# Optimization experiments

Hardware: AMD Instinct MI355X
Metric: run time of the kernel (lower is better)

Reference implementation:

```python
import jax, jax.numpy as jnp
import numpy as np

N_NODES = 50000
N_EDGES = 800000
N_ENTS = 200000
N_RELS = 500
D = 128


def setup_inputs() -> dict:
    key = jax.random.key(0)
    ks = jax.random.split(key, 9)
    return {
        "prev_ent_embs": jax.random.normal(ks[0], (N_ENTS, D), dtype=jnp.float32),
        "rel_embs": jax.random.normal(ks[1], (N_RELS, D), dtype=jnp.float32),
        "loop_weight": jax.random.normal(ks[2], (D, D), dtype=jnp.float32) * 0.1,
        "evolve_loop_weight": jax.random.normal(ks[3], (D, D), dtype=jnp.float32) * 0.1,
        "weight_neighbor": jax.random.normal(ks[4], (D, D), dtype=jnp.float32) * 0.1,
        "node_id": jax.random.randint(ks[5], (N_NODES,), 0, N_ENTS, dtype=jnp.int64) if jax.config.jax_enable_x64 else jax.random.randint(ks[5], (N_NODES,), 0, N_ENTS, dtype=jnp.int32),
        "src": jax.random.randint(ks[6], (N_EDGES,), 0, N_NODES, dtype=jnp.int32),
        "dst": jax.random.randint(ks[7], (N_EDGES,), 0, N_NODES, dtype=jnp.int32),
        "etype": jax.random.randint(ks[8], (N_EDGES,), 0, N_RELS, dtype=jnp.int32),
    }


def reference(prev_ent_embs, rel_embs, loop_weight, evolve_loop_weight,
              weight_neighbor, node_id, src, dst, etype):
    n_nodes = node_id.shape[0]
    # node features gathered from global entity table
    h = prev_ent_embs[node_id]                                    # [N, D]

    # per-edge message: (h[src] + rel[type]) @ W_neighbor
    msg = (h[src] + rel_embs[etype]) @ weight_neighbor            # [E, D]

    # scatter-sum into destination nodes
    agg = jax.ops.segment_sum(msg, dst, num_segments=n_nodes)     # [N, D]

    # in-degree and norm (apply_func: h * in_norm, standard 1/in_degree)
    deg = jax.ops.segment_sum(jnp.ones_like(dst, dtype=h.dtype), dst,
                              num_segments=n_nodes)               # [N]
    has_in = deg > 0
    in_norm = jnp.where(has_in, 1.0 / jnp.maximum(deg, 1.0), 0.0)[:, None]
    agg = agg * in_norm

    # self-loop: loop_weight where in_degree>0, evolve_loop_weight otherwise
    loop_msg = jnp.where(has_in[:, None], h @ loop_weight, h @ evolve_loop_weight)

    # activation (dropout=0 -> identity in eval)
    return jax.nn.relu(agg + loop_msg)
```

## Files before the change

### kernel.cpp

```cpp
#include <hip/hip_runtime.h>
#include <hip/hip_bf16.h>
#include <stdint.h>

#define N_NODES 50000
#define N_EDGES 800000
#define N_ENTS  200000
#define N_RELS  500
#define DIM     128

#define DEGS 32
#define CAP  64

#define ZERO_REC ((int)(50000u | (500u << 16)))

using f32x4  = __attribute__((ext_vector_type(4))) float;
using bf16x8 = __attribute__((ext_vector_type(8))) short;

static __device__ __forceinline__ ushort f_to_bf16(float f) {
    __hip_bfloat16 h = __float2bfloat16(f);
    return *reinterpret_cast<ushort*>(&h);
}
static __device__ __forceinline__ uint pack2(float a, float b) {
    return (uint)f_to_bf16(a) | ((uint)f_to_bf16(b) << 16);
}
static __device__ __forceinline__ float blo(uint u) { return __uint_as_float(u << 16); }
static __device__ __forceinline__ float bhi(uint u) { return __uint_as_float(u & 0xffff0000u); }

__global__ __launch_bounds__(256) void k_front(
        const float* __restrict__ prev, const int* __restrict__ node_id,
        ushort* __restrict__ afull,
        const int* __restrict__ dst, const int* __restrict__ src,
        const int* __restrict__ etype,
        int* __restrict__ deg, uint* __restrict__ srcpk,
        const float* __restrict__ rel, ushort* __restrict__ rel_bf,
        const float* __restrict__ Wn, const float* __restrict__ Wl,
        ushort* __restrict__ WfT) {
    int blk = blockIdx.x;
    if (blk < 3125) {
        int e = blk * 256 + threadIdx.x;
        if (e < N_EDGES) {
            int dn = dst[e];
            uint rec = (uint)src[e] | ((uint)etype[e] << 16);
            int r = atomicAdd(&deg[dn * DEGS], 1);
            if (r < CAP) srcpk[dn * CAP + r] = rec;
        }
    } else if (blk < 6250) {
        int i = (blk - 3125) * 256 + threadIdx.x;
        int row = i >> 4, c = (i & 15) * 8;
        int nid = node_id[row];
        const float* p = prev + (size_t)nid * DIM + c;
        float4 v0 = *(const float4*)p;
        float4 v1 = *(const float4*)(p + 4);
        uint4 w;
        w.x = pack2(v0.x, v0.y);
        w.y = pack2(v0.z, v0.w);
        w.z = pack2(v1.x, v1.y);
        w.w = pack2(v1.z, v1.w);
        *(uint4*)(afull + (size_t)row * 256 + 128 + c) = w;
    } else if (blk < 6504) {
        int i = (blk - 6250) * 256 + threadIdx.x;
        if (i < 128 * 256) {
            int n = i >> 8, k = i & 255;
            float v = (k < 128) ? Wn[k * 128 + n] : Wl[(k - 128) * 128 + n];
            WfT[i] = f_to_bf16(v);
        } else {
            int j = i - 128 * 256;
            if (j < N_RELS * 64) {
                float2 v = *(const float2*)(rel + j * 2);
                *(uint*)(rel_bf + j * 2) = pack2(v.x, v.y);
            }
        }
    } else {
        int t = threadIdx.x;
        if (t < 128)       ((uint*)(afull + (size_t)50000 * 256))[t] = 0u;
        else if (t < 192)  ((uint*)(rel_bf + 500 * 128))[t - 128]    = 0u;
    }
}

__global__ __launch_bounds__(256) void k_agg(ushort* __restrict__ afull,
                                             const ushort* __restrict__ rel_bf,
                                             const uint* __restrict__ srcpk,
                                             const int* __restrict__ deg) {
    int wave = threadIdx.x >> 6, lane = threadIdx.x & 63;
    int n = blockIdx.x * 4 + wave;
    if (n >= N_NODES) return;
    int d = deg[n * DEGS];
    int cnt = min(d, CAP);
    int g = lane >> 4, q = lane & 15;
    const ushort* hb = afull + 128 + q * 8;
    const ushort* rb = rel_bf + q * 8;
    float acc[8] = {0.f, 0.f, 0.f, 0.f, 0.f, 0.f, 0.f, 0.f};

#define ACC4(hv, rv)                                              \
    acc[0] += blo(hv.x) + blo(rv.x); acc[1] += bhi(hv.x) + bhi(rv.x); \
    acc[2] += blo(hv.y) + blo(rv.y); acc[3] += bhi(hv.y) + bhi(rv.y); \
    acc[4] += blo(hv.z) + blo(rv.z); acc[5] += bhi(hv.z) + bhi(rv.z); \
    acc[6] += blo(hv.w) + blo(rv.w); acc[7] += bhi(hv.w) + bhi(rv.w);

    int rec = (lane < cnt) ? (int)srcpk[n * CAP + lane] : ZERO_REC;
    for (int j = 0; j < cnt; j += 8) {
        uint e0 = (uint)__shfl(rec, j + g);
        uint e1 = (uint)__shfl(rec, j + 4 + g);
        uint4 h0 = *(const uint4*)(hb + (size_t)(e0 & 0xffffu) * 256);
        uint4 r0 = *(const uint4*)(rb + (e0 >> 16) * 128);
        uint4 h1 = *(const uint4*)(hb + (size_t)(e1 & 0xffffu) * 256);
        uint4 r1 = *(const uint4*)(rb + (e1 >> 16) * 128);
        ACC4(h0, r0);
        ACC4(h1, r1);
    }
#undef ACC4

#pragma unroll
    for (int i = 0; i < 8; i++) {
        acc[i] += __shfl_xor(acc[i], 16);
        acc[i] += __shfl_xor(acc[i], 32);
    }
    float norm = (d > 0) ? 1.0f / (float)d : 0.0f;
    if (g == 0) {
        uint4 w;
        w.x = pack2(acc[0] * norm, acc[1] * norm);
        w.y = pack2(acc[2] * norm, acc[3] * norm);
        w.z = pack2(acc[4] * norm, acc[5] * norm);
        w.w = pack2(acc[6] * norm, acc[7] * norm);
        *(uint4*)(afull + (size_t)n * 256 + q * 8) = w;
    }
}

#define LDSK 264
__global__ __launch_bounds__(256) void k_mm(const ushort* __restrict__ afull,
                                            const ushort* __restrict__ WfT,
                                            float* __restrict__ out) {
    __shared__ ushort wl[128 * LDSK];
    for (int idx = threadIdx.x; idx < 128 * 32; idx += 256) {
        int n = idx >> 5, p = idx & 31;
        uint4 v = *(const uint4*)(WfT + n * 256 + p * 8);
        *(uint4*)(&wl[n * LDSK + p * 8]) = v;
    }
    __syncthreads();

    int wave = threadIdx.x >> 6, lane = threadIdx.x & 63;
    int m = lane & 15, quad = lane >> 4;
    int rowBase = blockIdx.x * 128 + wave * 32;

    f32x4 acc[2][8];
#pragma unroll
    for (int rt = 0; rt < 2; rt++)
#pragma unroll
        for (int ct = 0; ct < 8; ct++) acc[rt][ct] = f32x4{0.f, 0.f, 0.f, 0.f};

    int r0 = rowBase + m;      if (r0 > N_NODES - 1) r0 = N_NODES - 1;
    int r1 = rowBase + 16 + m; if (r1 > N_NODES - 1) r1 = N_NODES - 1;
    const ushort* pa0 = afull + (size_t)r0 * 256 + quad * 8;
    const ushort* pa1 = afull + (size_t)r1 * 256 + quad * 8;

#pragma unroll
    for (int ks = 0; ks < 8; ks++) {
        bf16x8 a0 = *(const bf16x8*)(pa0 + ks * 32);
        bf16x8 a1 = *(const bf16x8*)(pa1 + ks * 32);
#pragma unroll
        for (int ct = 0; ct < 8; ct++) {
            bf16x8 b = *(const bf16x8*)(&wl[(ct * 16 + m) * LDSK + ks * 32 + quad * 8]);
            acc[0][ct] = __builtin_amdgcn_mfma_f32_16x16x32_bf16(a0, b, acc[0][ct], 0, 0, 0);
            acc[1][ct] = __builtin_amdgcn_mfma_f32_16x16x32_bf16(a1, b, acc[1][ct], 0, 0, 0);
        }
    }

#pragma unroll
    for (int rt = 0; rt < 2; rt++) {
        int rbase = rowBase + rt * 16 + quad * 4;
#pragma unroll
        for (int reg = 0; reg < 4; reg++) {
            int grow = rbase + reg;
            if (grow < N_NODES) {
#pragma unroll
                for (int ct = 0; ct < 8; ct++) {
                    float v = acc[rt][ct][reg];
                    out[(size_t)grow * 128 + ct * 16 + m] = v > 0.f ? v : 0.f;
                }
            }
        }
    }
}

__global__ __launch_bounds__(256) void k_fixup(const ushort* __restrict__ afull,
                                               const float* __restrict__ We,
                                               const int* __restrict__ deg,
                                               float* __restrict__ out) {
    int n = blockIdx.x * 256 + threadIdx.x;
    if (n >= N_NODES) return;
    if (deg[n * DEGS] != 0) return;
    for (int c = 0; c < 128; c++) {
        float a = 0.f;
        for (int k = 0; k < 128; k++) {
            float h = blo((uint)afull[(size_t)n * 256 + 128 + k]);
            a += h * We[k * 128 + c];
        }
        out[(size_t)n * 128 + c] = a > 0.f ? a : 0.f;
    }
}

extern "C" void kernel_launch(void* const* d_in, const int* in_sizes, int n_in,
                              void* d_out, int out_size, void* d_ws, size_t ws_size,
                              hipStream_t stream) {
    const float* prev  = (const float*)d_in[0];
    const float* rel   = (const float*)d_in[1];
    const float* Wl    = (const float*)d_in[2];
    const float* We    = (const float*)d_in[3];
    const float* Wn    = (const float*)d_in[4];
    const int* node_id = (const int*)d_in[5];
    const int* src     = (const int*)d_in[6];
    const int* dst     = (const int*)d_in[7];
    const int* etype   = (const int*)d_in[8];
    float* out = (float*)d_out;

    char* ws = (char*)d_ws;
    ushort* afull  = (ushort*)(ws);
    ushort* WfT    = (ushort*)(ws + 25600512);
    ushort* rel_bf = (ushort*)(ws + 25666048);
    int* deg       = (int*)(ws + 25794304);
    uint* srcpk    = (uint*)(ws + 32194304);

    hipMemsetAsync(deg, 0, 6400000, stream);
    k_front <<<6505,  256, 0, stream>>>(prev, node_id, afull, dst, src, etype,
                                        deg, srcpk, rel, rel_bf, Wn, Wl, WfT);
    k_agg   <<<12500, 256, 0, stream>>>(afull, rel_bf, srcpk, deg);
    k_mm    <<<391,   256, 0, stream>>>(afull, WfT, out);
    k_fixup <<<196,   256, 0, stream>>>(afull, We, deg, out);
}
```

Measured before the change: 242.2 us.

## Assign one node per 16-lane group in aggregation and fold fixup into matmul

The aggregation kernel now gives each 16-lane group its own destination node, so four nodes share a wave instead of one. Edge records are loaded in chunks of 16, which removes the cross-group shuffle reduction. The separate zero-in-degree fixup kernel is merged into the matmul launch as extra blocks, saving one kernel launch, and the matmul skips writing rows with no in-edges. The cost is uneven work inside a wave, since each group loops for its own node's degree, and the fixup blocks still run a slow scalar loop alongside the matmul blocks.

```diff
diff --git a/kernel.cpp b/kernel.cpp
--- a/kernel.cpp
+++ b/kernel.cpp
@@ -82,54 +82,66 @@
                                              const uint* __restrict__ srcpk,
                                              const int* __restrict__ deg) {
     int wave = threadIdx.x >> 6, lane = threadIdx.x & 63;
-    int n = blockIdx.x * 4 + wave;
-    if (n >= N_NODES) return;
+    int g = lane >> 4, q = lane & 15;
+    int n = blockIdx.x * 16 + wave * 4 + g;
     int d = deg[n * DEGS];
     int cnt = min(d, CAP);
-    int g = lane >> 4, q = lane & 15;
     const ushort* hb = afull + 128 + q * 8;
     const ushort* rb = rel_bf + q * 8;
     float acc[8] = {0.f, 0.f, 0.f, 0.f, 0.f, 0.f, 0.f, 0.f};
 
-#define ACC4(hv, rv)                                              \
+#define ACC4(hv, rv)                                                  \
     acc[0] += blo(hv.x) + blo(rv.x); acc[1] += bhi(hv.x) + bhi(rv.x); \
     acc[2] += blo(hv.y) + blo(rv.y); acc[3] += bhi(hv.y) + bhi(rv.y); \
     acc[4] += blo(hv.z) + blo(rv.z); acc[5] += bhi(hv.z) + bhi(rv.z); \
     acc[6] += blo(hv.w) + blo(rv.w); acc[7] += bhi(hv.w) + bhi(rv.w);
 
-    int rec = (lane < cnt) ? (int)srcpk[n * CAP + lane] : ZERO_REC;
-    for (int j = 0; j < cnt; j += 8) {
-        uint e0 = (uint)__shfl(rec, j + g);
-        uint e1 = (uint)__shfl(rec, j + 4 + g);
-        uint4 h0 = *(const uint4*)(hb + (size_t)(e0 & 0xffffu) * 256);
-        uint4 r0 = *(const uint4*)(rb + (e0 >> 16) * 128);
-        uint4 h1 = *(const uint4*)(hb + (size_t)(e1 & 0xffffu) * 256);
-        uint4 r1 = *(const uint4*)(rb + (e1 >> 16) * 128);
-        ACC4(h0, r0);
-        ACC4(h1, r1);
+    for (int b = 0; b < cnt; b += 16) {
+        int rec = (b + q < cnt) ? (int)srcpk[n * CAP + b + q] : ZERO_REC;
+        int jmax = min(16, cnt - b);
+        for (int j = 0; j < jmax; j += 2) {
+            uint e0 = (uint)__shfl(rec, (g << 4) + j);
+            uint e1 = (uint)__shfl(rec, (g << 4) + j + 1);
+            uint4 h0 = *(const uint4*)(hb + (size_t)(e0 & 0xffffu) * 256);
+            uint4 r0 = *(const uint4*)(rb + (e0 >> 16) * 128);
+            uint4 h1 = *(const uint4*)(hb + (size_t)(e1 & 0xffffu) * 256);
+            uint4 r1 = *(const uint4*)(rb + (e1 >> 16) * 128);
+            ACC4(h0, r0);
+            ACC4(h1, r1);
+        }
     }
 #undef ACC4
 
-#pragma unroll
-    for (int i = 0; i < 8; i++) {
-        acc[i] += __shfl_xor(acc[i], 16);
-        acc[i] += __shfl_xor(acc[i], 32);
-    }
     float norm = (d > 0) ? 1.0f / (float)d : 0.0f;
-    if (g == 0) {
-        uint4 w;
-        w.x = pack2(acc[0] * norm, acc[1] * norm);
-        w.y = pack2(acc[2] * norm, acc[3] * norm);
-        w.z = pack2(acc[4] * norm, acc[5] * norm);
-        w.w = pack2(acc[6] * norm, acc[7] * norm);
-        *(uint4*)(afull + (size_t)n * 256 + q * 8) = w;
-    }
+    uint4 w;
+    w.x = pack2(acc[0] * norm, acc[1] * norm);
+    w.y = pack2(acc[2] * norm, acc[3] * norm);
+    w.z = pack2(acc[4] * norm, acc[5] * norm);
+    w.w = pack2(acc[6] * norm, acc[7] * norm);
+    *(uint4*)(afull + (size_t)n * 256 + q * 8) = w;
 }
 
 #define LDSK 264
 __global__ __launch_bounds__(256) void k_mm(const ushort* __restrict__ afull,
                                             const ushort* __restrict__ WfT,
+                                            const int* __restrict__ deg,
+                                            const float* __restrict__ We,
                                             float* __restrict__ out) {
+    if (blockIdx.x >= 391) {
+        int n = (blockIdx.x - 391) * 256 + threadIdx.x;
+        if (n < N_NODES && deg[n * DEGS] == 0) {
+            for (int c = 0; c < 128; c++) {
+                float a = 0.f;
+                for (int k = 0; k < 128; k++) {
+                    float h = blo((uint)afull[(size_t)n * 256 + 128 + k]);
+                    a += h * We[k * 128 + c];
+                }
+                out[(size_t)n * 128 + c] = a > 0.f ? a : 0.f;
+            }
+        }
+        return;
+    }
+
     __shared__ ushort wl[128 * LDSK];
     for (int idx = threadIdx.x; idx < 128 * 32; idx += 256) {
         int n = idx >> 5, p = idx & 31;
@@ -171,7 +183,7 @@
 #pragma unroll
         for (int reg = 0; reg < 4; reg++) {
             int grow = rbase + reg;
-            if (grow < N_NODES) {
+            if (grow < N_NODES && deg[grow * DEGS] != 0) {
 #pragma unroll
                 for (int ct = 0; ct < 8; ct++) {
                     float v = acc[rt][ct][reg];
@@ -179,23 +191,6 @@
                 }
             }
         }
-    }
-}
-
-__global__ __launch_bounds__(256) void k_fixup(const ushort* __restrict__ afull,
-                                               const float* __restrict__ We,
-                                               const int* __restrict__ deg,
-                                               float* __restrict__ out) {
-    int n = blockIdx.x * 256 + threadIdx.x;
-    if (n >= N_NODES) return;
-    if (deg[n * DEGS] != 0) return;
-    for (int c = 0; c < 128; c++) {
-        float a = 0.f;
-        for (int k = 0; k < 128; k++) {
-            float h = blo((uint)afull[(size_t)n * 256 + 128 + k]);
-            a += h * We[k * 128 + c];
-        }
-        out[(size_t)n * 128 + c] = a > 0.f ? a : 0.f;
     }
 }
 
@@ -221,9 +216,8 @@
     uint* srcpk    = (uint*)(ws + 32194304);
 
     hipMemsetAsync(deg, 0, 6400000, stream);
-    k_front <<<6505,  256, 0, stream>>>(prev, node_id, afull, dst, src, etype,
-                                        deg, srcpk, rel, rel_bf, Wn, Wl, WfT);
-    k_agg   <<<12500, 256, 0, stream>>>(afull, rel_bf, srcpk, deg);
-    k_mm    <<<391,   256, 0, stream>>>(afull, WfT, out);
-    k_fixup <<<196,   256, 0, stream>>>(afull, We, deg, out);
-}
+    k_front <<<6505, 256, 0, stream>>>(prev, node_id, afull, dst, src, etype,
+                                       deg, srcpk, rel, rel_bf, Wn, Wl, WfT);
+    k_agg   <<<3125, 256, 0, stream>>>(afull, rel_bf, srcpk, deg);
+    k_mm    <<<587,  256, 0, stream>>>(afull, WfT, deg, We, out);
+}
```

Result: no change. 243.0 us (+0.3%).
